# Optimization experiments

Hardware: AMD Instinct MI355X
Metric: run time of the kernel (lower is better)

Reference implementation:

```python
import jax, jax.numpy as jnp
import numpy as np

LN_EPS = 1e-5


def setup_inputs() -> dict:
    key = jax.random.key(0)
    ks = jax.random.split(key, 4)
    B, N, C, K = 512, 100, 256, 3
    query = jax.random.normal(ks[0], (B, N, C), dtype=jnp.float32)
    value = jax.random.normal(ks[1], (B, N, C), dtype=jnp.float32)
    # nn.Linear(C, N+K): weight stored as [out,in] in torch; here use [in,out]
    W_wl = jax.random.normal(ks[2], (C, N + K), dtype=jnp.float32) / np.sqrt(C)
    b_wl = jax.random.normal(ks[3], (N + K,), dtype=jnp.float32) * 0.01
    ln_gamma = jnp.ones((C,), dtype=jnp.float32)
    ln_beta = jnp.zeros((C,), dtype=jnp.float32)
    return {"query": query, "value": value, "W_wl": W_wl, "b_wl": b_wl,
            "ln_gamma": ln_gamma, "ln_beta": ln_beta}


def reference(query, value, W_wl, b_wl, ln_gamma, ln_beta):
    B, N, C = query.shape
    K = W_wl.shape[1] - N
    # dynamic conv weights from query: [B, N, K] depthwise + [B, N, N] pointwise
    dy = jnp.einsum('bnc,ck->bnk', query, W_wl) + b_wl
    dw = dy[:, :, :K]          # depthwise kernels, one per (b, proposal)
    pw = dy[:, :, K:]          # pointwise mixing matrix [B, N, N]
    # depthwise conv1d along C with 'same' padding (cross-correlation like torch)
    pad_l = (K - 1) // 2
    pad_r = K - 1 - pad_l
    vp = jnp.pad(value, ((0, 0), (0, 0), (pad_l, pad_r)))
    depth = jnp.zeros_like(value)
    for k in range(K):  # K is tiny (3): static unrolled loop
        depth = depth + dw[:, :, k:k + 1] * vp[:, :, k:k + C]
    depth = jax.nn.relu(depth)
    # pointwise conv (kernel size 1) == per-sample NxN mix over proposals
    out = jnp.einsum('bnm,bmc->bnc', pw, depth)
    # LayerNorm over C
    mu = jnp.mean(out, axis=-1, keepdims=True)
    var = jnp.var(out, axis=-1, keepdims=True)
    out = (out - mu) * jax.lax.rsqrt(var + LN_EPS) * ln_gamma + ln_beta
    return out
```

## Files before the change

### kernel.cpp

```cpp
#include <hip/hip_runtime.h>

#define NN 100
#define CC 256
#define NKK 103
#define LDT 136
#define OTS 260
#define LDW 136

typedef __bf16 bf16;
typedef __bf16 bf16x8 __attribute__((ext_vector_type(8)));
typedef float f32x4 __attribute__((ext_vector_type(4)));


__global__ void wl_transpose(const float* __restrict__ W, bf16* __restrict__ Wt)
{
    int idx = blockIdx.x * 256 + threadIdx.x;
    if (idx < NKK * CC) {
        int ka = idx >> 8;
        int k  = idx & 255;
        Wt[ka * CC + k] = (bf16)W[k * NKK + ka];
    }
}

__global__ __launch_bounds__(256, 4)
void gemm1(const float* __restrict__ query, const bf16* __restrict__ Wt,
           const float* __restrict__ bwl, float* __restrict__ out)
{
    __shared__ __align__(16) bf16 ST[4][16][LDW];
    const int t    = threadIdx.x;
    const int w    = t >> 6;
    const int lane = t & 63;
    const int ln16 = lane & 15;
    const int g    = lane >> 4;
    const int hi8  = g * 8;
    const int R0   = blockIdx.x * 64 + w * 16;

    const float* qr = query + (size_t)(R0 + ln16) * CC;
    bf16x8 qfr[8];
    #pragma unroll
    for (int f = 0; f < 8; ++f) {
        const int col = f * 32 + hi8;
        f32x4 a0 = *(const f32x4*)(qr + col);
        f32x4 a1 = *(const f32x4*)(qr + col + 4);
        #pragma unroll
        for (int i = 0; i < 4; ++i) { qfr[f][i] = (bf16)a0[i]; qfr[f][i + 4] = (bf16)a1[i]; }
    }

    f32x4 acc[7];
    #pragma unroll
    for (int J = 0; J < 7; ++J) acc[J] = (f32x4){0.f, 0.f, 0.f, 0.f};

    #pragma unroll
    for (int J = 0; J < 7; ++J) {
        const int rB = (J * 16 + ln16 < NKK) ? (J * 16 + ln16) : (NKK - 1);
        const bf16* wr = Wt + rB * CC;
        #pragma unroll
        for (int f = 0; f < 8; ++f) {
            bf16x8 bv = *(const bf16x8*)(wr + f * 32 + hi8);
            acc[J] = __builtin_amdgcn_mfma_f32_16x16x32_bf16(qfr[f], bv, acc[J], 0, 0, 0);
        }
    }

    #pragma unroll
    for (int J = 0; J < 7; ++J) {
        int kap = J * 16 + ln16;
        float bw = (kap < NKK) ? bwl[kap] : 0.f;
        #pragma unroll
        for (int r = 0; r < 4; ++r) {
            float v = acc[J][r] + bw;
            int row = g * 4 + r;
            if (kap >= 3 && kap < NKK) {
                ST[w][row][kap - 3] = (bf16)v;
            } else if (J == 0 && kap < 3) {
                int nf  = R0 + row;
                int bbb = nf / 100, nnr = nf - bbb * 100;
                out[(size_t)bbb * 25600 + 6400 + nnr * 4 + kap] = v;
            }
        }
    }
    #pragma unroll
    for (int p = 0; p < 4; ++p) {
        int row = p * 4 + g;
        int nf  = R0 + row;
        int bbb = nf / 100, nnr = nf - bbb * 100;
        bf16x8 vrow = *(const bf16x8*)&ST[w][row][ln16 * 8];
        *(bf16x8*)((bf16*)(out + (size_t)bbb * 25600) + nnr * 128 + ln16 * 8) = vrow;
    }
}

__global__ __launch_bounds__(512, 4)
void conv_gemm2_ln(const float* __restrict__ value,
                   const float* __restrict__ gamma,
                   const float* __restrict__ beta,
                   float* __restrict__ out)
{
    __shared__ __align__(16) char SMEM[71232];
    bf16* depthT = (bf16*)SMEM;
    float (*DWs)[4] = (float(*)[4])(SMEM + 69632);
    float* OT = (float*)SMEM;

    const int t    = threadIdx.x;
    const int w    = t >> 6;
    const int lane = t & 63;
    const int ln16 = lane & 15;
    const int g    = lane >> 4;
    const int hi8  = g * 8;
    const int b    = blockIdx.x;
    const int cb   = w * 16 + ln16;

    float* ob = out + (size_t)b * 25600;
    const bf16*  pwb = (const bf16*)ob;
    const float* vb  = value + (size_t)b * NN * CC;

    if (t < 400) ((float*)DWs)[t] = ob[6400 + t];
    float xv[2][8];
    #pragma unroll
    for (int s = 0; s < 2; ++s)
        #pragma unroll
        for (int j = 0; j < 8; ++j)
            xv[s][j] = vb[(hi8 + j) * CC + cb + 128 * s];
    __syncthreads();

    #pragma unroll
    for (int ks = 0; ks < 4; ++ks) {
        if (ks) {
            #pragma unroll
            for (int s = 0; s < 2; ++s)
                #pragma unroll
                for (int j = 0; j < 8; ++j) {
                    int m = ks * 32 + hi8 + j;
                    xv[s][j] = (m < NN) ? vb[m * CC + cb + 128 * s] : 0.f;
                }
        }
        bf16x8 dv[2];
        #pragma unroll
        for (int j = 0; j < 8; ++j) {
            int  m  = ks * 32 + hi8 + j;
            bool mv = (m < NN);
            int  mc = mv ? m : (NN - 1);
            float w0 = DWs[mc][0], w1 = DWs[mc][1], w2 = DWs[mc][2];
            #pragma unroll
            for (int s = 0; s < 2; ++s) {
                int c = cb + 128 * s;
                float x0 = xv[s][j];
                float xm = __shfl(x0, (lane - 1) & 63);
                float xp = __shfl(x0, (lane + 1) & 63);
                if (ln16 == 0)  xm = (mv && c > 0)      ? vb[m * CC + c - 1] : 0.f;
                if (ln16 == 15) xp = (mv && c + 1 < CC) ? vb[m * CC + c + 1] : 0.f;
                float d = w0 * xm + w1 * x0 + w2 * xp;
                dv[s][j] = (bf16)(mv ? fmaxf(d, 0.f) : 0.f);
            }
        }
        #pragma unroll
        for (int s = 0; s < 2; ++s)
            *(bf16x8*)&depthT[(cb + 128 * s) * LDT + ks * 32 + hi8] = dv[s];
    }

    bf16x8 av[4];
    if (w < 7) {
        const int arow = (w * 16 + ln16 < NN) ? (w * 16 + ln16) : (NN - 1);
        #pragma unroll
        for (int ks = 0; ks < 4; ++ks)
            av[ks] = *(const bf16x8*)(pwb + arow * 128 + ks * 32 + hi8);
    }
    __syncthreads();

    f32x4 acc[16];
    #pragma unroll
    for (int ct = 0; ct < 16; ++ct) acc[ct] = (f32x4){0.f, 0.f, 0.f, 0.f};
    float mu[4], rs[4];

    if (w < 7) {
        #pragma unroll
        for (int j = 0; j < 8; ++j)
            av[3][j] = (96 + hi8 + j < NN) ? av[3][j] : (bf16)0.f;

        #pragma unroll
        for (int ct = 0; ct < 16; ++ct) {
            #pragma unroll
            for (int ks = 0; ks < 4; ++ks) {
                bf16x8 bv = *(const bf16x8*)&depthT[(ct * 16 + ln16) * LDT + ks * 32 + hi8];
                acc[ct] = __builtin_amdgcn_mfma_f32_16x16x32_bf16(av[ks], bv, acc[ct], 0, 0, 0);
            }
        }
        #pragma unroll
        for (int r = 0; r < 4; ++r) {
            float s1 = 0.f, s2 = 0.f;
            #pragma unroll
            for (int ct = 0; ct < 16; ++ct) { float a = acc[ct][r]; s1 += a; s2 += a * a; }
            #pragma unroll
            for (int mk = 1; mk < 16; mk <<= 1) {
                s1 += __shfl_xor(s1, mk);
                s2 += __shfl_xor(s2, mk);
            }
            float m_ = s1 * (1.f / 256.f);
            float v_ = s2 * (1.f / 256.f) - m_ * m_;
            mu[r] = m_;
            rs[r] = rsqrtf(fmaxf(v_, 0.f) + 1e-5f);
        }
    }
    __syncthreads();

    #pragma unroll
    for (int h = 0; h < 2; ++h) {
        if (w >= 4 * h && w < 4 * h + 4 && w < 7) {
            const int slot = w - 4 * h;
            #pragma unroll
            for (int ct = 0; ct < 16; ++ct) {
                const float gmv = gamma[ct * 16 + ln16], btv = beta[ct * 16 + ln16];
                #pragma unroll
                for (int r = 0; r < 4; ++r)
                    OT[(slot * 16 + g * 4 + r) * OTS + ct * 16 + ln16] =
                        (acc[ct][r] - mu[r]) * rs[r] * gmv + btv;
            }
        }
        __syncthreads();
        const int rows = h ? 36 : 64;
        #pragma unroll
        for (int p = 0; p < 8; ++p) {
            int idx = p * 512 + t;
            if (idx < rows * 64) {
                int row = idx >> 6, c4 = (idx & 63) << 2;
                *(f32x4*)(ob + (size_t)(64 * h + row) * CC + c4) = *(const f32x4*)&OT[row * OTS + c4];
            }
        }
        if (h == 0) __syncthreads();
    }
}

extern "C" void kernel_launch(void* const* d_in, const int* in_sizes, int n_in,
                              void* d_out, int out_size, void* d_ws, size_t ws_size,
                              hipStream_t stream) {
    const float* query = (const float*)d_in[0];
    const float* value = (const float*)d_in[1];
    const float* W     = (const float*)d_in[2];
    const float* bwl   = (const float*)d_in[3];
    const float* gamma = (const float*)d_in[4];
    const float* beta  = (const float*)d_in[5];
    float* out = (float*)d_out;
    bf16* Wt = (bf16*)d_ws;

    wl_transpose<<<dim3((NKK * CC + 255) / 256), dim3(256), 0, stream>>>(W, Wt);
    gemm1<<<dim3(800), dim3(256), 0, stream>>>(query, Wt, bwl, out);
    conv_gemm2_ln<<<dim3(512), dim3(512), 0, stream>>>(value, gamma, beta, out);
}
```

Measured before the change: 186.1 us.

## Prepack weights in MFMA fragment order and stage query through LDS

The weight-prep kernel now writes W in the exact per-lane MFMA B-fragment order, so each lane in gemm1 does one contiguous 16-byte load per fragment instead of strided row reads. Query rows are loaded coalesced across the wave, converted to bf16 and staged in shared memory, then read back as A fragments. The DW scratch stride in the conv kernel is padded to 5 floats to avoid LDS bank conflicts. This adds extra block barriers and a larger shared buffer in gemm1.

```diff
diff --git a/kernel.cpp b/kernel.cpp
--- a/kernel.cpp
+++ b/kernel.cpp
@@ -5,28 +5,34 @@
 #define NKK 103
 #define LDT 136
 #define OTS 260
-#define LDW 136
+#define LQS 264
 
 typedef __bf16 bf16;
+typedef __bf16 bf16x4 __attribute__((ext_vector_type(4)));
 typedef __bf16 bf16x8 __attribute__((ext_vector_type(8)));
 typedef float f32x4 __attribute__((ext_vector_type(4)));
 
 
-__global__ void wl_transpose(const float* __restrict__ W, bf16* __restrict__ Wt)
+__global__ void wl_frag(const float* __restrict__ W, bf16* __restrict__ Wt2)
 {
     int idx = blockIdx.x * 256 + threadIdx.x;
-    if (idx < NKK * CC) {
-        int ka = idx >> 8;
-        int k  = idx & 255;
-        Wt[ka * CC + k] = (bf16)W[k * NKK + ka];
+    if (idx < 7 * 8 * 64 * 8) {
+        int j    = idx & 7;
+        int lane = (idx >> 3) & 63;
+        int f    = (idx >> 9) & 7;
+        int J    = idx >> 12;
+        int ka   = J * 16 + (lane & 15);
+        if (ka > NKK - 1) ka = NKK - 1;
+        int k    = f * 32 + ((lane >> 4) << 3) + j;
+        Wt2[idx] = (bf16)W[k * NKK + ka];
     }
 }
 
 __global__ __launch_bounds__(256, 4)
-void gemm1(const float* __restrict__ query, const bf16* __restrict__ Wt,
+void gemm1(const float* __restrict__ query, const bf16* __restrict__ Wt2,
            const float* __restrict__ bwl, float* __restrict__ out)
 {
-    __shared__ __align__(16) bf16 ST[4][16][LDW];
+    __shared__ __align__(16) bf16 ST[4][16][LQS];
     const int t    = threadIdx.x;
     const int w    = t >> 6;
     const int lane = t & 63;
@@ -35,16 +41,21 @@
     const int hi8  = g * 8;
     const int R0   = blockIdx.x * 64 + w * 16;
 
-    const float* qr = query + (size_t)(R0 + ln16) * CC;
+    const float* qb = query + (size_t)R0 * CC;
+    #pragma unroll
+    for (int p = 0; p < 16; ++p) {
+        f32x4 v = *(const f32x4*)(qb + p * CC + lane * 4);
+        bf16x4 s;
+        #pragma unroll
+        for (int i = 0; i < 4; ++i) s[i] = (bf16)v[i];
+        *(bf16x4*)&ST[w][p][lane * 4] = s;
+    }
+    __syncthreads();
+
     bf16x8 qfr[8];
     #pragma unroll
-    for (int f = 0; f < 8; ++f) {
-        const int col = f * 32 + hi8;
-        f32x4 a0 = *(const f32x4*)(qr + col);
-        f32x4 a1 = *(const f32x4*)(qr + col + 4);
-        #pragma unroll
-        for (int i = 0; i < 4; ++i) { qfr[f][i] = (bf16)a0[i]; qfr[f][i + 4] = (bf16)a1[i]; }
-    }
+    for (int f = 0; f < 8; ++f)
+        qfr[f] = *(const bf16x8*)&ST[w][ln16][f * 32 + hi8];
 
     f32x4 acc[7];
     #pragma unroll
@@ -52,14 +63,14 @@
 
     #pragma unroll
     for (int J = 0; J < 7; ++J) {
-        const int rB = (J * 16 + ln16 < NKK) ? (J * 16 + ln16) : (NKK - 1);
-        const bf16* wr = Wt + rB * CC;
+        const bf16* wb = Wt2 + (size_t)(J * 8) * 512 + lane * 8;
         #pragma unroll
         for (int f = 0; f < 8; ++f) {
-            bf16x8 bv = *(const bf16x8*)(wr + f * 32 + hi8);
+            bf16x8 bv = *(const bf16x8*)(wb + f * 512);
             acc[J] = __builtin_amdgcn_mfma_f32_16x16x32_bf16(qfr[f], bv, acc[J], 0, 0, 0);
         }
     }
+    __syncthreads();
 
     #pragma unroll
     for (int J = 0; J < 7; ++J) {
@@ -94,9 +105,9 @@
                    const float* __restrict__ beta,
                    float* __restrict__ out)
 {
-    __shared__ __align__(16) char SMEM[71232];
+    __shared__ __align__(16) char SMEM[71632];
     bf16* depthT = (bf16*)SMEM;
-    float (*DWs)[4] = (float(*)[4])(SMEM + 69632);
+    float (*DWs)[5] = (float(*)[5])(SMEM + 69632);
     float* OT = (float*)SMEM;
 
     const int t    = threadIdx.x;
@@ -112,7 +123,7 @@
     const bf16*  pwb = (const bf16*)ob;
     const float* vb  = value + (size_t)b * NN * CC;
 
-    if (t < 400) ((float*)DWs)[t] = ob[6400 + t];
+    if (t < 400) DWs[t >> 2][t & 3] = ob[6400 + t];
     float xv[2][8];
     #pragma unroll
     for (int s = 0; s < 2; ++s)
@@ -238,9 +249,9 @@
     const float* gamma = (const float*)d_in[4];
     const float* beta  = (const float*)d_in[5];
     float* out = (float*)d_out;
-    bf16* Wt = (bf16*)d_ws;
-
-    wl_transpose<<<dim3((NKK * CC + 255) / 256), dim3(256), 0, stream>>>(W, Wt);
-    gemm1<<<dim3(800), dim3(256), 0, stream>>>(query, Wt, bwl, out);
+    bf16* Wt2 = (bf16*)d_ws;
+
+    wl_frag<<<dim3(112), dim3(256), 0, stream>>>(W, Wt2);
+    gemm1<<<dim3(800), dim3(256), 0, stream>>>(query, Wt2, bwl, out);
     conv_gemm2_ln<<<dim3(512), dim3(512), 0, stream>>>(value, gamma, beta, out);
 }
```

After: 173.9 us. 6.5% less time.
